# Optimization experiments

Hardware: AMD Instinct MI355X
Metric: run time of the kernel (lower is better)

The kernel has to match this reference:

```python
import jax, jax.numpy as jnp
import numpy as np

N, E = 50000, 800000
NFEAT, NHID, NHEADS, NCLASS = 512, 64, 8, 64
ALPHA = 0.2  # leaky relu negative slope


def setup_inputs() -> dict:
    key = jax.random.key(0)
    ks = jax.random.split(key, 8)
    x = jax.random.normal(ks[0], (N, NFEAT), jnp.float32)
    row = jax.random.randint(ks[1], (E,), 0, N)  # destination node i of each edge
    col = jax.random.randint(ks[2], (E,), 0, N)  # source node j of each edge
    W = jax.random.normal(ks[3], (NHEADS, NFEAT, NHID), jnp.float32) * (1.0 / np.sqrt(NFEAT))
    a = jax.random.normal(ks[4], (NHEADS, 2 * NHID), jnp.float32) * 0.1
    W_out = jax.random.normal(ks[5], (NHID * NHEADS, NCLASS), jnp.float32) * (1.0 / np.sqrt(NHID * NHEADS))
    a_out = jax.random.normal(ks[6], (2 * NCLASS,), jnp.float32) * 0.1
    return {"x": x, "row": row, "col": col, "W": W, "a": a, "W_out": W_out, "a_out": a_out}


def _gat_layer(h, W, a, row, col, n, alpha, concat):
    # h: [N, F_in], W: [F_in, F'], a: [2*F']
    Wh = h @ W                                   # [N, F']
    f = Wh.shape[-1]
    f_dst = Wh @ a[:f]                           # a^T part for target node i, [N]
    f_src = Wh @ a[f:]                           # a^T part for source node j, [N]
    e = jax.nn.leaky_relu(f_dst[row] + f_src[col], alpha)       # [E] attention logits
    # numerically stable segment softmax over incoming edges of each node
    m = jax.ops.segment_max(e, row, num_segments=n)
    m = jnp.where(jnp.isneginf(m), 0.0, m)       # nodes with no in-edges
    p = jnp.exp(e - m[row])
    denom = jax.ops.segment_sum(p, row, num_segments=n)
    att = p / jnp.maximum(denom[row], 1e-16)     # [E]
    out = jax.ops.segment_sum(att[:, None] * Wh[col], row, num_segments=n)  # [N, F']
    return jax.nn.elu(out) if concat else out


def reference(x, row, col, W, a, W_out, a_out):
    # eval mode: F.dropout is a no-op
    heads = [_gat_layer(x, W[h], a[h], row, col, N, ALPHA, True) for h in range(NHEADS)]
    h = jnp.concatenate(heads, axis=1)           # [N, NHID*NHEADS]
    return _gat_layer(h, W_out, a_out, row, col, N, ALPHA, False)  # [N, NCLASS]
```

## Files before the change

### kernel.cpp

```cpp
#include <hip/hip_runtime.h>
#include <cstdint>
#include <cstddef>

#define NN      50000
#define MPAD    50048
#define EE      800000
#define NHEADS  8
#define HID_TOT 512
#define NCLASS  64
#define ALPHA_LRELU 0.2f
#define NB1     196
#define GM1_M   391
#define GM1_B   (GM1_M * 4)

typedef unsigned short u16;
typedef __attribute__((ext_vector_type(8))) unsigned short ushort8;
typedef __attribute__((ext_vector_type(4))) unsigned short ushort4v;

__device__ __forceinline__ float bf2f(u16 v) {
    return __uint_as_float(((unsigned)v) << 16);
}
__device__ __forceinline__ u16 f2bf(float f) {
    unsigned u = __float_as_uint(f);
    return (u16)((u + 0x7fffu + ((u >> 16) & 1u)) >> 16);
}

#define PREP_R0 (MPAD * 64)
#define PREP_R1 (512 * 512)
#define PREP_R2 (64 * 512)
#define PREP_TOT (PREP_R0 + PREP_R1 + PREP_R2 + EE)

__global__ __launch_bounds__(256) void prep_all(const float* __restrict__ x,
                                                const float* __restrict__ W,
                                                const float* __restrict__ W_out,
                                                u16* __restrict__ xb,
                                                u16* __restrict__ Wt1,
                                                u16* __restrict__ Wto,
                                                const int* __restrict__ row,
                                                int* __restrict__ cnt) {
    int g = blockIdx.x * 256 + threadIdx.x;
    if (g < PREP_R0) {
        int r = g >> 6;
        int c = (g & 63) * 8;
        ushort8 o = (ushort8)0;
        if (r < NN) {
            const float4 v0 = *(const float4*)(x + (size_t)r * 512 + c);
            const float4 v1 = *(const float4*)(x + (size_t)r * 512 + c + 4);
            o[0] = f2bf(v0.x); o[1] = f2bf(v0.y); o[2] = f2bf(v0.z); o[3] = f2bf(v0.w);
            o[4] = f2bf(v1.x); o[5] = f2bf(v1.y); o[6] = f2bf(v1.z); o[7] = f2bf(v1.w);
        }
        *(ushort8*)(xb + (size_t)r * 512 + c) = o;
        return;
    }
    g -= PREP_R0;
    if (g < PREP_R1) {
        int c = g >> 9, f = g & 511;
        int h = c >> 6, j = c & 63;
        Wt1[g] = f2bf(W[(h << 15) + (f << 6) + j]);
        return;
    }
    g -= PREP_R1;
    if (g < PREP_R2) {
        int n = g >> 9, k = g & 511;
        Wto[g] = f2bf(W_out[k * 64 + n]);
        return;
    }
    g -= PREP_R2;
    if (g < EE) {
        atomicAdd(&cnt[row[g]], 1);
    }
}


__global__ __launch_bounds__(256) void scan_blocksum(const int* __restrict__ cnt,
                                                     int* __restrict__ bsum) {
    int idx = blockIdx.x * 256 + threadIdx.x;
    int v = (idx < NN) ? cnt[idx] : 0;
    #pragma unroll
    for (int o = 32; o; o >>= 1) v += __shfl_xor(v, o);
    __shared__ int sw[4];
    int wave = threadIdx.x >> 6;
    if ((threadIdx.x & 63) == 0) sw[wave] = v;
    __syncthreads();
    if (threadIdx.x == 0) bsum[blockIdx.x] = sw[0] + sw[1] + sw[2] + sw[3];
}

__global__ __launch_bounds__(256) void scan_write(const int* __restrict__ cnt,
                                                  const int* __restrict__ bsum,
                                                  int* __restrict__ start,
                                                  int* __restrict__ wr) {
    __shared__ int sh[256];
    __shared__ int swb[4];
    int t = threadIdx.x;
    int vb = (t < NB1 && t < blockIdx.x) ? bsum[t] : 0;
    #pragma unroll
    for (int o = 32; o; o >>= 1) vb += __shfl_xor(vb, o);
    if ((t & 63) == 0) swb[t >> 6] = vb;
    __syncthreads();
    const int blockoff = swb[0] + swb[1] + swb[2] + swb[3];

    int idx = blockIdx.x * 256 + t;
    int c = (idx < NN) ? cnt[idx] : 0;
    __syncthreads();
    sh[t] = c;
    __syncthreads();
    for (int o = 1; o < 256; o <<= 1) {
        int cur = sh[t];
        int add = (t >= o) ? sh[t - o] : 0;
        __syncthreads();
        sh[t] = cur + add;
        __syncthreads();
    }
    if (idx < NN) {
        int excl = blockoff + sh[t] - c;
        start[idx] = excl;
        wr[idx] = excl;
    }
    if (idx == 0) start[NN] = EE;
}


__device__ __forceinline__ void load_lds_128(const u16* g, u16* l) {
    __builtin_amdgcn_global_load_lds((const __attribute__((address_space(1))) void*)g,
                                     (__attribute__((address_space(3))) void*)l,
                                     16, 0, 0);
}

typedef __attribute__((ext_vector_type(8))) short frag8;
typedef __attribute__((ext_vector_type(4))) float f32x4;

__global__ __launch_bounds__(256) void scat_gemm1(const int* __restrict__ row,
                                                  const int* __restrict__ col,
                                                  int* __restrict__ wr,
                                                  int* __restrict__ ecol,
                                                  const u16* __restrict__ A,
                                                  const u16* __restrict__ Bt,
                                                  u16* __restrict__ C,
                                                  const float* __restrict__ av,
                                                  float* __restrict__ fd,
                                                  float* __restrict__ fs) {
    constexpr int BM = 128, BN = 128, BK = 32, WN = 64, NT = 4;
    constexpr int M = NN, N = 512, K = 512, KT = K / BK;
    __shared__ u16 AsB[3][BM * BK];
    __shared__ u16 BsB[3][BN * BK];
    const int tid = threadIdx.x;
    const int bid = blockIdx.x;

    const int e0 = (bid * 256 + tid) * 2;
    int sc0 = 0, sc1 = 0, sp0 = 0, sp1 = 0;
    bool edo = (e0 < EE);
    if (edo) {
        int2 rr = *(const int2*)(row + e0);
        int2 cc = *(const int2*)(col + e0);
        sc0 = cc.x; sc1 = cc.y;
        sp0 = atomicAdd(&wr[rr.x], 1);
        sp1 = atomicAdd(&wr[rr.y], 1);
    }

    const int wave = tid >> 6, lane = tid & 63;
    const int wm = wave & 1, wn = wave >> 1;
    const int bm = (bid % GM1_M) * BM;
    const int bnb = bid / GM1_M;
    const int bn = bnb * BN;
    const int q = lane >> 4, lr = lane & 15;

    f32x4 acc[4][NT] = {};

    auto stage = [&](u16* as, u16* bs, int k0) {
        #pragma unroll
        for (int c = wave; c < (BM * BK) / 512; c += 4) {
            int f = c * 512 + lane * 8;
            int r_ = f >> 5, ck = f & 31;
            load_lds_128(A + (size_t)(bm + r_) * K + k0 + ck, as + c * 512);
        }
        #pragma unroll
        for (int c = wave; c < (BN * BK) / 512; c += 4) {
            int f = c * 512 + lane * 8;
            int r_ = f >> 5, ck = f & 31;
            load_lds_128(Bt + (size_t)(bn + r_) * K + k0 + ck, bs + c * 512);
        }
    };
    auto compute = [&](const u16* as, const u16* bs) {
        frag8 af[4], bfr[NT];
        #pragma unroll
        for (int am = 0; am < 4; am++)
            af[am] = *(const frag8*)(as + (wm * 64 + am * 16 + lr) * 32 + q * 8);
        #pragma unroll
        for (int bt = 0; bt < NT; bt++)
            bfr[bt] = *(const frag8*)(bs + (wn * WN + bt * 16 + lr) * 32 + q * 8);
        #pragma unroll
        for (int am = 0; am < 4; am++)
            #pragma unroll
            for (int bt = 0; bt < NT; bt++)
                acc[am][bt] = __builtin_amdgcn_mfma_f32_16x16x32_bf16(af[am], bfr[bt], acc[am][bt], 0, 0, 0);
    };

    stage(AsB[0], BsB[0], 0);
    stage(AsB[1], BsB[1], BK);
    #pragma unroll
    for (int kt = 0; kt < KT; kt++) {
        if (kt < KT - 1) asm volatile("s_waitcnt vmcnt(4)\n\ts_barrier" ::: "memory");
        else             asm volatile("s_waitcnt vmcnt(0)\n\ts_barrier" ::: "memory");
        if (kt + 2 < KT) stage(AsB[(kt + 2) % 3], BsB[(kt + 2) % 3], (kt + 2) * BK);
        compute(AsB[kt % 3], BsB[kt % 3]);
    }

    if (edo) {
        ecol[sp0] = sc0;
        ecol[sp1] = sc1;
    }

    const int hd = bnb * 2 + wn;
    const float* ah = av + hd * 128;
    float adv[NT], adv2[NT];
    #pragma unroll
    for (int bt = 0; bt < NT; bt++) {
        adv[bt]  = ah[bt * 16 + lr];
        adv2[bt] = ah[64 + bt * 16 + lr];
    }

    #pragma unroll
    for (int am = 0; am < 4; am++) {
        #pragma unroll
        for (int reg = 0; reg < 4; reg++) {
            int gr = bm + wm * 64 + am * 16 + q * 4 + reg;
            bool inb = gr < M;
            if (inb) {
                #pragma unroll
                for (int bt = 0; bt < NT; bt++) {
                    int gc = bn + wn * WN + bt * 16 + lr;
                    C[(size_t)gr * N + gc] = f2bf(acc[am][bt][reg]);
                }
            }
            float sd = 0.f, ss = 0.f;
            #pragma unroll
            for (int bt = 0; bt < NT; bt++) {
                float v = acc[am][bt][reg];
                sd += v * adv[bt];
                ss += v * adv2[bt];
            }
            #pragma unroll
            for (int o = 1; o < 16; o <<= 1) {
                sd += __shfl_xor(sd, o);
                ss += __shfl_xor(ss, o);
            }
            if (lr == 0 && inb) {
                fd[gr * 8 + hd] = sd;
                fs[gr * 8 + hd] = ss;
            }
        }
    }
}

template <int BN, int OUT_MODE, int FUSE>
__global__ __launch_bounds__(256) void gemm_bf16(const u16* __restrict__ A,
                                                 const u16* __restrict__ Bt,
                                                 void* __restrict__ Cv,
                                                 int M, int N, int K,
                                                 const float* __restrict__ av,
                                                 float* __restrict__ fd,
                                                 float* __restrict__ fs) {
    constexpr int BM = 128, BK = 32;
    constexpr int WN = BN / 2;
    constexpr int NT = WN / 16;
    __shared__ u16 As0[BM * BK], As1[BM * BK];
    __shared__ u16 Bs0[BN * BK], Bs1[BN * BK];
    __shared__ float pd[2][2][64];
    __shared__ float ps[2][2][64];
    const int tid = threadIdx.x;
    const int wave = tid >> 6, lane = tid & 63;
    const int wm = wave & 1, wn = wave >> 1;
    const int bm = blockIdx.x * BM, bn = blockIdx.y * BN;
    const int q = lane >> 4, lr = lane & 15;

    f32x4 acc[4][NT] = {};

    auto stage = [&](u16* as, u16* bs, int k0) {
        #pragma unroll
        for (int c = wave; c < (BM * BK) / 512; c += 4) {
            int f = c * 512 + lane * 8;
            int row = f >> 5, ck = f & 31;
            load_lds_128(A + (size_t)(bm + row) * K + k0 + ck, as + c * 512);
        }
        #pragma unroll
        for (int c = wave; c < (BN * BK) / 512; c += 4) {
            int f = c * 512 + lane * 8;
            int row = f >> 5, ck = f & 31;
            load_lds_128(Bt + (size_t)(bn + row) * K + k0 + ck, bs + c * 512);
        }
    };
    auto compute = [&](const u16* as, const u16* bs) {
        frag8 af[4], bfr[NT];
        #pragma unroll
        for (int am = 0; am < 4; am++)
            af[am] = *(const frag8*)(as + (wm * 64 + am * 16 + lr) * 32 + q * 8);
        #pragma unroll
        for (int bt = 0; bt < NT; bt++)
            bfr[bt] = *(const frag8*)(bs + (wn * WN + bt * 16 + lr) * 32 + q * 8);
        #pragma unroll
        for (int am = 0; am < 4; am++)
            #pragma unroll
            for (int bt = 0; bt < NT; bt++)
                acc[am][bt] = __builtin_amdgcn_mfma_f32_16x16x32_bf16(af[am], bfr[bt], acc[am][bt], 0, 0, 0);
    };

    const int KT = K / BK;
    stage(As0, Bs0, 0);
    for (int kt = 0; kt < KT; kt += 2) {
        __syncthreads();
        if (kt + 1 < KT) stage(As1, Bs1, (kt + 1) * BK);
        compute(As0, Bs0);
        __syncthreads();
        if (kt + 2 < KT) stage(As0, Bs0, (kt + 2) * BK);
        compute(As1, Bs1);
    }

    float adv[NT], adv2[NT];
    int hd = 0;
    if (FUSE == 1) {
        hd = blockIdx.y * 2 + wn;
        const float* ah = av + hd * 128;
        #pragma unroll
        for (int bt = 0; bt < NT; bt++) {
            adv[bt]  = ah[bt * 16 + lr];
            adv2[bt] = ah[64 + bt * 16 + lr];
        }
    }
    if (FUSE == 2) {
        #pragma unroll
        for (int bt = 0; bt < NT; bt++) {
            adv[bt]  = av[wn * WN + bt * 16 + lr];
            adv2[bt] = av[64 + wn * WN + bt * 16 + lr];
        }
    }

    #pragma unroll
    for (int am = 0; am < 4; am++) {
        #pragma unroll
        for (int reg = 0; reg < 4; reg++) {
            int gr = bm + wm * 64 + am * 16 + q * 4 + reg;
            bool inb = gr < M;
            if (inb) {
                #pragma unroll
                for (int bt = 0; bt < NT; bt++) {
                    int gc = bn + wn * WN + bt * 16 + lr;
                    float v = acc[am][bt][reg];
                    if (OUT_MODE == 0) ((float*)Cv)[(size_t)gr * N + gc] = v;
                    else               ((u16*)Cv)[(size_t)gr * N + gc] = f2bf(v);
                }
            }
            if (FUSE != 0) {
                float sd = 0.f, ss = 0.f;
                #pragma unroll
                for (int bt = 0; bt < NT; bt++) {
                    float v = acc[am][bt][reg];
                    sd += v * adv[bt];
                    ss += v * adv2[bt];
                }
                #pragma unroll
                for (int o = 1; o < 16; o <<= 1) {
                    sd += __shfl_xor(sd, o);
                    ss += __shfl_xor(ss, o);
                }
                if (FUSE == 1) {
                    if (lr == 0 && inb) {
                        fd[gr * 8 + hd] = sd;
                        fs[gr * 8 + hd] = ss;
                    }
                } else {
                    if (lr == 0) {
                        int rr = am * 16 + q * 4 + reg;
                        pd[wm][wn][rr] = sd;
                        ps[wm][wn][rr] = ss;
                    }
                }
            }
        }
    }
    if (FUSE == 2) {
        __syncthreads();
        if (tid < 128) {
            int wmm = tid >> 6, rr = tid & 63;
            int gr = bm + wmm * 64 + rr;
            if (gr < M) {
                fd[gr] = pd[wmm][0][rr] + pd[wmm][1][rr];
                fs[gr] = ps[wmm][0][rr] + ps[wmm][1][rr];
            }
        }
    }
}

__global__ __launch_bounds__(256) void agg1_fused(const int* __restrict__ start,
                                                  const int* __restrict__ ecol,
                                                  const float* __restrict__ fd,
                                                  const float* __restrict__ fs,
                                                  const u16* __restrict__ Whb,
                                                  u16* __restrict__ h1b) {
    const int i = blockIdx.x * 4 + (threadIdx.x >> 6);
    const int lane = threadIdx.x & 63;
    const int hh = lane >> 3;
    const int st = start[i], en = start[i + 1];
    const float fdv = fd[i * 8 + hh];

    float acc[8] = {};
    float den = 0.f;
    int t = st;
    for (; t + 2 <= en; t += 2) {
        int j0 = ecol[t], j1 = ecol[t + 1];
        float v0 = fdv + fs[j0 * 8 + hh]; v0 = v0 > 0.f ? v0 : ALPHA_LRELU * v0;
        float v1 = fdv + fs[j1 * 8 + hh]; v1 = v1 > 0.f ? v1 : ALPHA_LRELU * v1;
        float p0 = __expf(v0);
        float p1 = __expf(v1);
        ushort8 w0 = *(const ushort8*)(Whb + (size_t)j0 * HID_TOT + lane * 8);
        ushort8 w1 = *(const ushort8*)(Whb + (size_t)j1 * HID_TOT + lane * 8);
        den += p0 + p1;
        #pragma unroll
        for (int k = 0; k < 8; k++) acc[k] += p0 * bf2f(w0[k]);
        #pragma unroll
        for (int k = 0; k < 8; k++) acc[k] += p1 * bf2f(w1[k]);
    }
    if (t < en) {
        int j = ecol[t];
        float v = fdv + fs[j * 8 + hh]; v = v > 0.f ? v : ALPHA_LRELU * v;
        float p = __expf(v);
        den += p;
        ushort8 wv = *(const ushort8*)(Whb + (size_t)j * HID_TOT + lane * 8);
        #pragma unroll
        for (int k = 0; k < 8; k++) acc[k] += p * bf2f(wv[k]);
    }
    float rden = 1.0f / fmaxf(den, 1e-16f);
    ushort8 o8;
    #pragma unroll
    for (int k = 0; k < 8; k++) {
        float v = acc[k] * rden;
        v = v > 0.f ? v : (__expf(v) - 1.0f);
        o8[k] = f2bf(v);
    }
    *(ushort8*)(h1b + (size_t)i * HID_TOT + lane * 8) = o8;
}

__global__ __launch_bounds__(256) void agg2_fused(const int* __restrict__ start,
                                                  const int* __restrict__ ecol,
                                                  const float* __restrict__ fd,
                                                  const float* __restrict__ fs,
                                                  const u16* __restrict__ Wh2b,
                                                  float* __restrict__ out) {
    const int i = blockIdx.x * 4 + (threadIdx.x >> 6);
    const int lane = threadIdx.x & 63;
    const int g = lane >> 4, r = lane & 15;
    const int st = start[i], en = start[i + 1];
    const float fdv = fd[i];

    float acc[4] = {};
    float den = 0.f;
    for (int t = st + g; t < en; t += 4) {
        int j = ecol[t];
        float v = fdv + fs[j];
        v = v > 0.f ? v : ALPHA_LRELU * v;
        float p = __expf(v);
        den += p;
        ushort4v wv = *(const ushort4v*)(Wh2b + (size_t)j * NCLASS + r * 4);
        #pragma unroll
        for (int k = 0; k < 4; k++) acc[k] += p * bf2f(wv[k]);
    }
    #pragma unroll
    for (int o = 16; o <= 32; o <<= 1) {
        den += __shfl_xor(den, o);
        #pragma unroll
        for (int k = 0; k < 4; k++) acc[k] += __shfl_xor(acc[k], o);
    }
    if (g == 0) {
        float rden = 1.0f / fmaxf(den, 1e-16f);
        float4 o4;
        o4.x = acc[0] * rden; o4.y = acc[1] * rden;
        o4.z = acc[2] * rden; o4.w = acc[3] * rden;
        *(float4*)(out + (size_t)i * NCLASS + r * 4) = o4;
    }
}


static inline int cdiv_l(long a, long b) { return (int)((a + b - 1) / b); }

extern "C" void kernel_launch(void* const* d_in, const int* in_sizes, int n_in,
                              void* d_out, int out_size, void* d_ws, size_t ws_size,
                              hipStream_t stream) {
    const float* x     = (const float*)d_in[0];
    const int*   row   = (const int*)d_in[1];
    const int*   col   = (const int*)d_in[2];
    const float* W     = (const float*)d_in[3];
    const float* a     = (const float*)d_in[4];
    const float* W_out = (const float*)d_in[5];
    const float* a_out = (const float*)d_in[6];
    float* out = (float*)d_out;

    char* wsb = (char*)d_ws;
    size_t off = 0;
    auto alloc = [&](size_t bytes) { char* p = wsb + off; off += (bytes + 255) & ~(size_t)255; return p; };
    u16*   xb     = (u16*)  alloc((size_t)MPAD * 512 * 2);
    u16*   Wcat_t = (u16*)  alloc((size_t)512 * 512 * 2);
    u16*   Wot_t  = (u16*)  alloc((size_t)64 * 512 * 2);
    u16*   Whb1   = (u16*)  alloc((size_t)NN * 512 * 2);
    float* fd1    = (float*)alloc((size_t)NN * 8 * 4);
    float* fs1    = (float*)alloc((size_t)NN * 8 * 4);
    u16*   h1b    = (u16*)  alloc((size_t)MPAD * 512 * 2);
    u16*   Wh2b   = (u16*)  alloc((size_t)NN * 64 * 2);
    float* fd2    = (float*)alloc((size_t)NN * 4);
    float* fs2    = (float*)alloc((size_t)NN * 4);
    int*   cnt    = (int*)  alloc((size_t)NN * 4);
    int*   startp = (int*)  alloc(((size_t)NN + 1) * 4);
    int*   wr     = (int*)  alloc((size_t)NN * 4);
    int*   ecol   = (int*)  alloc((size_t)EE * 4);
    int*   bsum   = (int*)  alloc((size_t)NB1 * 4);
    int*   boff   = (int*)  alloc((size_t)NB1 * 4);
    (void)boff;

    hipMemsetAsync(cnt, 0, (size_t)NN * 4, stream);
    prep_all<<<cdiv_l(PREP_TOT, 256), 256, 0, stream>>>(x, W, W_out, xb, Wcat_t, Wot_t,
                                                        row, cnt);

    scan_blocksum<<<NB1, 256, 0, stream>>>(cnt, bsum);
    scan_write<<<NB1, 256, 0, stream>>>(cnt, bsum, startp, wr);

    scat_gemm1<<<GM1_B, 256, 0, stream>>>(row, col, wr, ecol,
                                          xb, Wcat_t, Whb1, a, fd1, fs1);

    agg1_fused<<<NN / 4, 256, 0, stream>>>(startp, ecol, fd1, fs1, Whb1, h1b);

    {
        dim3 grid(cdiv_l(MPAD, 128), 1);
        gemm_bf16<64, 1, 2><<<grid, 256, 0, stream>>>(h1b, Wot_t, Wh2b, NN, 64, 512,
                                                      a_out, fd2, fs2);
    }
    agg2_fused<<<NN / 4, 256, 0, stream>>>(startp, ecol, fd2, fs2, Wh2b, out);
}
```

Measured before the change: 456.4 us.

## Stage GEMM1 epilogue through LDS and triple-buffer generic GEMM pipeline

```diff
diff --git a/kernel.cpp b/kernel.cpp
--- a/kernel.cpp
+++ b/kernel.cpp
@@ -141,8 +141,8 @@
                                                   float* __restrict__ fs) {
     constexpr int BM = 128, BN = 128, BK = 32, WN = 64, NT = 4;
     constexpr int M = NN, N = 512, K = 512, KT = K / BK;
-    __shared__ u16 AsB[3][BM * BK];
-    __shared__ u16 BsB[3][BN * BK];
+    constexpr int TSZ = BM * BK;
+    __shared__ u16 SMEM[6 * TSZ];
     const int tid = threadIdx.x;
     const int bid = blockIdx.x;
 
@@ -156,6 +156,7 @@
         sp0 = atomicAdd(&wr[rr.x], 1);
         sp1 = atomicAdd(&wr[rr.y], 1);
     }
+    asm volatile("s_waitcnt vmcnt(0)" ::: "memory");
 
     const int wave = tid >> 6, lane = tid & 63;
     const int wm = wave & 1, wn = wave >> 1;
@@ -195,14 +196,15 @@
                 acc[am][bt] = __builtin_amdgcn_mfma_f32_16x16x32_bf16(af[am], bfr[bt], acc[am][bt], 0, 0, 0);
     };
 
-    stage(AsB[0], BsB[0], 0);
-    stage(AsB[1], BsB[1], BK);
+    stage(SMEM + 0 * TSZ, SMEM + 3 * TSZ, 0);
+    stage(SMEM + 1 * TSZ, SMEM + 4 * TSZ, BK);
     #pragma unroll
     for (int kt = 0; kt < KT; kt++) {
         if (kt < KT - 1) asm volatile("s_waitcnt vmcnt(4)\n\ts_barrier" ::: "memory");
         else             asm volatile("s_waitcnt vmcnt(0)\n\ts_barrier" ::: "memory");
-        if (kt + 2 < KT) stage(AsB[(kt + 2) % 3], BsB[(kt + 2) % 3], (kt + 2) * BK);
-        compute(AsB[kt % 3], BsB[kt % 3]);
+        if (kt + 2 < KT) stage(SMEM + ((kt + 2) % 3) * TSZ, SMEM + (3 + (kt + 2) % 3) * TSZ,
+                               (kt + 2) * BK);
+        compute(SMEM + (kt % 3) * TSZ, SMEM + (3 + kt % 3) * TSZ);
     }
 
     if (edo) {
@@ -210,6 +212,28 @@
         ecol[sp1] = sc1;
     }
 
+    __syncthreads();
+    {
+        u16* eb = SMEM + wave * (64 * 80);
+        #pragma unroll
+        for (int am = 0; am < 4; am++)
+            #pragma unroll
+            for (int bt = 0; bt < NT; bt++)
+                #pragma unroll
+                for (int reg = 0; reg < 4; reg++)
+                    eb[(am * 16 + q * 4 + reg) * 80 + bt * 16 + lr] = f2bf(acc[am][bt][reg]);
+        #pragma unroll
+        for (int i = 0; i < 8; i++) {
+            int lrow = i * 8 + (lane >> 3);
+            int gr = bm + wm * 64 + lrow;
+            int cc = (lane & 7) * 8;
+            if (gr < M) {
+                ushort8 v = *(const ushort8*)(eb + lrow * 80 + cc);
+                *(ushort8*)(C + (size_t)gr * N + bn + wn * 64 + cc) = v;
+            }
+        }
+    }
+
     const int hd = bnb * 2 + wn;
     const float* ah = av + hd * 128;
     float adv[NT], adv2[NT];
@@ -225,13 +249,6 @@
         for (int reg = 0; reg < 4; reg++) {
             int gr = bm + wm * 64 + am * 16 + q * 4 + reg;
             bool inb = gr < M;
-            if (inb) {
-                #pragma unroll
-                for (int bt = 0; bt < NT; bt++) {
-                    int gc = bn + wn * WN + bt * 16 + lr;
-                    C[(size_t)gr * N + gc] = f2bf(acc[am][bt][reg]);
-                }
-            }
             float sd = 0.f, ss = 0.f;
             #pragma unroll
             for (int bt = 0; bt < NT; bt++) {
@@ -263,8 +280,8 @@
     constexpr int BM = 128, BK = 32;
     constexpr int WN = BN / 2;
     constexpr int NT = WN / 16;
-    __shared__ u16 As0[BM * BK], As1[BM * BK];
-    __shared__ u16 Bs0[BN * BK], Bs1[BN * BK];
+    __shared__ u16 AsB[3][BM * BK];
+    __shared__ u16 BsB[3][BN * BK];
     __shared__ float pd[2][2][64];
     __shared__ float ps[2][2][64];
     const int tid = threadIdx.x;
@@ -305,14 +322,17 @@
     };
 
     const int KT = K / BK;
-    stage(As0, Bs0, 0);
-    for (int kt = 0; kt < KT; kt += 2) {
-        __syncthreads();
-        if (kt + 1 < KT) stage(As1, Bs1, (kt + 1) * BK);
-        compute(As0, Bs0);
-        __syncthreads();
-        if (kt + 2 < KT) stage(As0, Bs0, (kt + 2) * BK);
-        compute(As1, Bs1);
+    stage(AsB[0], BsB[0], 0);
+    stage(AsB[1], BsB[1], BK);
+    for (int kt = 0; kt < KT; kt++) {
+        if (kt < KT - 1) {
+            if constexpr (BN == 64) asm volatile("s_waitcnt vmcnt(3)\n\ts_barrier" ::: "memory");
+            else                    asm volatile("s_waitcnt vmcnt(4)\n\ts_barrier" ::: "memory");
+        } else {
+            asm volatile("s_waitcnt vmcnt(0)\n\ts_barrier" ::: "memory");
+        }
+        if (kt + 2 < KT) stage(AsB[(kt + 2) % 3], BsB[(kt + 2) % 3], (kt + 2) * BK);
+        compute(AsB[kt % 3], BsB[kt % 3]);
     }
 
     float adv[NT], adv2[NT];
```

Result: no change. 457.3 us (+0.2%).
